# Performance work log

Measured on AMD Instinct MI355X. Metric: run time of the kernel, lower is better.

Reference implementation:

```python
import jax, jax.numpy as jnp
import numpy as np

D = 2048   # embed_dim
E = 128    # expand_ratio = head dim
H = D // E # num heads = 16
C = 64     # chunk size for the chunked linear-attention scan
EPS = 1e-6


def setup_inputs() -> dict:
    key = jax.random.key(0)
    ks = jax.random.split(key, 6)
    b, n = 2, 2048
    s = 0.02
    x = jax.random.normal(ks[0], (b, n, D), jnp.float32)
    Wq = (jax.random.normal(ks[1], (D, D), jnp.float32) * s)
    Wk = (jax.random.normal(ks[2], (D, D), jnp.float32) * s)
    Wv = (jax.random.normal(ks[3], (D, D), jnp.float32) * s)
    Wf = (jax.random.normal(ks[4], (D, H), jnp.float32) * s)
    Wo = (jax.random.normal(ks[5], (D, D), jnp.float32) * s)
    norm_w = jnp.ones((D,), jnp.float32)
    return {"x": x, "Wq": Wq, "Wk": Wk, "Wv": Wv, "Wf": Wf, "Wo": Wo, "norm_w": norm_w}


def _lightning_scalar_decay(q, k, v, ld):
    # q,k,v: [b,n,H,E], ld: [b,n,H] log decay per head per step.
    # Recurrence: S_t = exp(ld_t) * S_{t-1} + k_t^T v_t ; o_t = q_t @ S_t
    b, n, h, e = q.shape
    nc = n // C
    qc = q.reshape(b, nc, C, h, e)
    kc = k.reshape(b, nc, C, h, e)
    vc = v.reshape(b, nc, C, h, e)
    ldc = ld.reshape(b, nc, C, h)
    cum = jnp.cumsum(ldc, axis=2)          # inclusive within-chunk log decay [b,nc,C,h]
    tot = cum[:, :, -1, :]                 # [b,nc,h]

    # intra-chunk: scores[i,j] = (q_i . k_j) * exp(L_i - L_j), j <= i
    Lh = cum.transpose(0, 1, 3, 2)         # [b,nc,h,C]
    decay = jnp.exp(Lh[..., :, None] - Lh[..., None, :])  # [b,nc,h,C,C]
    mask = jnp.tril(jnp.ones((C, C), bool))
    scores = jnp.einsum('bmihe,bmjhe->bmhij', qc, kc) * decay
    scores = jnp.where(mask, scores, 0.0)
    o_intra = jnp.einsum('bmhij,bmjhe->bmihe', scores, vc)

    # inter-chunk: carried recurrent state S [b,h,e,e]
    def step(S, inp):
        q_c, k_c, v_c, cum_c, tot_c = inp  # [b,C,h,e],...,[b,C,h],[b,h]
        o = jnp.einsum('bihe,bhef->bihf', q_c * jnp.exp(cum_c)[..., None], S)
        kd = k_c * jnp.exp(tot_c[:, None, :] - cum_c)[..., None]
        S_new = S * jnp.exp(tot_c)[:, :, None, None] + jnp.einsum('bihe,bihf->bhef', kd, v_c)
        return S_new, o

    xs = (qc.transpose(1, 0, 2, 3, 4), kc.transpose(1, 0, 2, 3, 4),
          vc.transpose(1, 0, 2, 3, 4), cum.transpose(1, 0, 2, 3), tot.transpose(1, 0, 2))
    S0 = jnp.zeros((b, h, e, e), q.dtype)
    S_final, o_inter = jax.lax.scan(step, S0, xs)
    o_inter = o_inter.transpose(1, 0, 2, 3, 4)  # [b,nc,C,h,e]
    return (o_intra + o_inter).reshape(b, n, h * e), S_final


def reference(x, Wq, Wk, Wv, Wf, Wo, norm_w):
    b, n, d = x.shape
    q = jax.nn.silu(x @ Wq).reshape(b, n, H, E)
    k = jax.nn.silu(x @ Wk).reshape(b, n, H, E)
    v = (x @ Wv).reshape(b, n, H, E)
    ld = jax.nn.log_sigmoid(x @ Wf)  # [b,n,H]
    o, _ = _lightning_scalar_decay(q, k, v, ld)
    # RMSNorm over full embed dim
    o = o * jax.lax.rsqrt(jnp.mean(o * o, axis=-1, keepdims=True) + EPS) * norm_w
    return o @ Wo
```

## Files before the change

kernel.cpp:

```cpp
#include <hip/hip_runtime.h>
#include <hip/hip_bf16.h>
#include <stdint.h>

#define D_ 2048
#define E_ 128
#define H_ 16
#define NB_ 2
#define NSEQ_ 2048
#define NTOK_ 4096
#define NCH_ 32

typedef short bf16s;
typedef __attribute__((ext_vector_type(8))) short bf16x8;
typedef __attribute__((ext_vector_type(4))) float f32x4;

__device__ __forceinline__ short f2b(float f) {
  __hip_bfloat16 h = __float2bfloat16(f);
  return *reinterpret_cast<short*>(&h);
}
__device__ __forceinline__ float b2f(short s) {
  __hip_bfloat16 h;
  *reinterpret_cast<short*>(&h) = s;
  return __bfloat162float(h);
}

__device__ __forceinline__ void gload_lds16(const void* g, void* l) {
  __builtin_amdgcn_global_load_lds(
      (__attribute__((address_space(1))) void*)(const_cast<void*>(g)),
      (__attribute__((address_space(3))) void*)(l), 16, 0, 0);
}

__global__ __launch_bounds__(256)
void cvt_bf16(const float* __restrict__ x, bf16s* __restrict__ y) {
  const size_t i = (size_t)blockIdx.x * 256 + threadIdx.x;
  const float4 a = ((const float4*)x)[i * 2];
  const float4 b = ((const float4*)x)[i * 2 + 1];
  bf16x8 o;
  o[0] = f2b(a.x); o[1] = f2b(a.y); o[2] = f2b(a.z); o[3] = f2b(a.w);
  o[4] = f2b(b.x); o[5] = f2b(b.y); o[6] = f2b(b.z); o[7] = f2b(b.w);
  *(bf16x8*)&y[i * 8] = o;
}

__global__ __launch_bounds__(256)
void transpose_w(const float* __restrict__ Wq, const float* __restrict__ Wk,
                 const float* __restrict__ Wv, const float* __restrict__ Wo,
                 bf16s* __restrict__ WqT, bf16s* __restrict__ WkT,
                 bf16s* __restrict__ WvT, bf16s* __restrict__ WoT) {
  const float* src; bf16s* dst;
  if (blockIdx.z == 0)      { src = Wq; dst = WqT; }
  else if (blockIdx.z == 1) { src = Wk; dst = WkT; }
  else if (blockIdx.z == 2) { src = Wv; dst = WvT; }
  else                      { src = Wo; dst = WoT; }
  __shared__ float tile[64][65];
  const int n0 = blockIdx.x * 64, k0 = blockIdx.y * 64;
  const int t = threadIdx.x;
  const int tr = t >> 6, tc = t & 63;
#pragma unroll
  for (int rr = 0; rr < 16; ++rr) {
    const int row = rr * 4 + tr;
    tile[row][tc] = src[(size_t)(k0 + row) * D_ + n0 + tc];
  }
  __syncthreads();
#pragma unroll
  for (int rr = 0; rr < 16; ++rr) {
    const int row = rr * 4 + tr;
    dst[(size_t)(n0 + row) * D_ + k0 + tc] = f2b(tile[tc][row]);
  }
}

__global__ __launch_bounds__(256)
void ld_gemm(const float* __restrict__ x, const float* __restrict__ Wf,
             float* __restrict__ ldb) {
  const int t = threadIdx.x;
  const int col = t & 15;
  const int tok = blockIdx.x * 16 + (t >> 4);
  const float4* xr = (const float4*)(x + (size_t)tok * D_);
  float s = 0.f;
#pragma unroll 4
  for (int kk = 0; kk < D_ / 4; ++kk) {
    const float4 xv = xr[kk];
    const int k4 = kk * 4;
    s += xv.x * Wf[(k4 + 0) * H_ + col];
    s += xv.y * Wf[(k4 + 1) * H_ + col];
    s += xv.z * Wf[(k4 + 2) * H_ + col];
    s += xv.w * Wf[(k4 + 3) * H_ + col];
  }
  const float m = fminf(s, 0.f);
  ldb[(size_t)tok * H_ + col] = m - log1pf(__expf(-fabsf(s)));
}

template <typename OT>
__device__ __forceinline__ void gemm_body(const bf16s* __restrict__ A,
                                          const bf16s* __restrict__ Bt,
                                          OT* __restrict__ Cm, int bm, int bn,
                                          int act) {
  constexpr int BK = 64;
  __shared__ bf16s As[128 * BK];
  __shared__ bf16s Bs[128 * BK];
  const int t = threadIdx.x;
  const int w = t >> 6, l = t & 63;
  const int wm = w >> 1, wn = w & 1;
  const int lr = l & 15, lk = l >> 4;
  const int sr8 = l >> 3, sc = l & 7;
  const int cs = sc ^ sr8;
  f32x4 acc[4][4] = {};

  const size_t abase = (size_t)(bm * 128) * D_;
  const size_t bbase = (size_t)(bn * 128) * D_;

  for (int k0 = 0; k0 < D_; k0 += BK) {
    __syncthreads();
#pragma unroll
    for (int j = 0; j < 4; ++j) {
      const int row = w * 32 + j * 8;
      gload_lds16(&A[abase + (size_t)(row + sr8) * D_ + k0 + cs * 8],
                  &As[row * BK]);
      gload_lds16(&Bt[bbase + (size_t)(row + sr8) * D_ + k0 + cs * 8],
                  &Bs[row * BK]);
    }
    __syncthreads();
    bf16x8 af[4][2], bfr[4][2];
#pragma unroll
    for (int tm = 0; tm < 4; ++tm) {
      const int row = wm * 64 + tm * 16 + lr;
#pragma unroll
      for (int ks = 0; ks < 2; ++ks)
        af[tm][ks] =
            *(const bf16x8*)&As[row * BK + ((ks * 4 + lk) ^ (row & 7)) * 8];
    }
#pragma unroll
    for (int tn = 0; tn < 4; ++tn) {
      const int row = wn * 64 + tn * 16 + lr;
#pragma unroll
      for (int ks = 0; ks < 2; ++ks)
        bfr[tn][ks] =
            *(const bf16x8*)&Bs[row * BK + ((ks * 4 + lk) ^ (row & 7)) * 8];
    }
#pragma unroll
    for (int ks = 0; ks < 2; ++ks)
#pragma unroll
      for (int tm = 0; tm < 4; ++tm)
#pragma unroll
        for (int tn = 0; tn < 4; ++tn)
          acc[tm][tn] = __builtin_amdgcn_mfma_f32_16x16x32_bf16(
              af[tm][ks], bfr[tn][ks], acc[tm][tn], 0, 0, 0);
  }

#pragma unroll
  for (int tm = 0; tm < 4; ++tm) {
    const int rowb = bm * 128 + wm * 64 + tm * 16 + lk * 4;
#pragma unroll
    for (int tn = 0; tn < 4; ++tn) {
      const int col = bn * 128 + wn * 64 + tn * 16 + lr;
#pragma unroll
      for (int r = 0; r < 4; ++r) {
        float vv = acc[tm][tn][r];
        if (act) vv = vv / (1.f + __expf(-vv));
        if constexpr (sizeof(OT) == 2)
          Cm[(size_t)(rowb + r) * D_ + col] = f2b(vv);
        else
          Cm[(size_t)(rowb + r) * D_ + col] = vv;
      }
    }
  }
}

__global__ __launch_bounds__(256)
void gemm_qkv(const bf16s* __restrict__ xb, const bf16s* __restrict__ WqT,
              const bf16s* __restrict__ WkT, const bf16s* __restrict__ WvT,
              bf16s* __restrict__ qb, bf16s* __restrict__ kb,
              bf16s* __restrict__ vb) {
  const int orig = blockIdx.x;
  const int lin = (orig & 7) * 192 + (orig >> 3);
  const int bm = lin & 31;
  const int bnz = lin >> 5;
  const int z = bnz >> 4, bn = bnz & 15;
  const bf16s* Bt; bf16s* out; int act;
  if (z == 0)      { Bt = WqT; out = qb; act = 1; }
  else if (z == 1) { Bt = WkT; out = kb; act = 1; }
  else             { Bt = WvT; out = vb; act = 0; }
  gemm_body<bf16s>(xb, Bt, out, bm, bn, act);
}

__global__ __launch_bounds__(256)
void gemm_out(const bf16s* __restrict__ A, const bf16s* __restrict__ Bt,
              float* __restrict__ out) {
  const int orig = blockIdx.x;
  const int lin = (orig & 7) * 64 + (orig >> 3);
  const int bm = lin & 31;
  const int bn = lin >> 5;
  gemm_body<float>(A, Bt, out, bm, bn, 0);
}

__global__ __launch_bounds__(256)
void chunk_state(const bf16s* __restrict__ k, const bf16s* __restrict__ v,
                 const float* __restrict__ ldp, bf16s* __restrict__ Mbuf,
                 float* __restrict__ totb) {
  const int c = blockIdx.x, bh = blockIdx.y;
  const int b = bh >> 4, h = bh & 15;
  const int t = threadIdx.x;
  const int w = t >> 6, l = t & 63;
  const int lr = l & 15, lk = l >> 4;

  __shared__ bf16s Kt[64 * 128];
  __shared__ bf16s Vn[64 * 128];
  __shared__ bf16s KdT[128 * 64];
  __shared__ bf16s VtT[128 * 64];
  __shared__ float cumS[64];
  char* cKt = (char*)Kt; char* cVn = (char*)Vn;
  char* cKdT = (char*)KdT; char* cVtT = (char*)VtT;

  const size_t grow0 = (size_t)b * NSEQ_ + c * 64;
#pragma unroll
  for (int j = 0; j < 4; ++j) {
    const int lrow = w * 16 + j * 4 + (l >> 4);
    const int ck = (l & 15) ^ (lrow & 7);
    const size_t goff = (grow0 + lrow) * D_ + h * E_ + ck * 8;
    const int lbase = (w * 16 + j * 4) * 128;
    gload_lds16(&k[goff], &Kt[lbase]);
    gload_lds16(&v[goff], &Vn[lbase]);
  }
  if (w == 0) {
    float val = ldp[(grow0 + l) * H_ + h];
#pragma unroll
    for (int off = 1; off < 64; off <<= 1) {
      float pv = __shfl_up(val, off);
      if (l >= off) val += pv;
    }
    cumS[l] = val;
  }
  __syncthreads();
  const float tot = cumS[63];
  if (t == 0) totb[bh * NCH_ + c] = tot;

#pragma unroll
  for (int it = 0; it < 4; ++it) {
    const int task = t + it * 256;
    const int i = task >> 4, cx = task & 15;
    const int sb = i * 256 + ((cx * 16) ^ ((i & 7) << 4));
    bf16x8 vv = *(const bf16x8*)(cVn + sb);
    bf16x8 kk8 = *(const bf16x8*)(cKt + sb);
    const float sE = __expf(tot - cumS[i]);
#pragma unroll
    for (int jj = 0; jj < 8; ++jj) {
      const int e = cx * 8 + jj;
      const int db = e * 128 + ((i * 2) ^ ((e & 7) << 4));
      *(bf16s*)(cVtT + db) = vv[jj];
      *(bf16s*)(cKdT + db) = f2b(b2f(kk8[jj]) * sE);
    }
  }
  __syncthreads();

  const int wm = w >> 1, wn = w & 1;
  f32x4 acc[4][4] = {};
#pragma unroll
  for (int kk2 = 0; kk2 < 2; ++kk2) {
    const int cb = (kk2 * 32 + lk * 8) * 2;
    bf16x8 af[4], bfr[4];
#pragma unroll
    for (int tm = 0; tm < 4; ++tm) {
      const int fr = wm * 64 + tm * 16 + lr;
      af[tm] = *(const bf16x8*)(cVtT + fr * 128 + (cb ^ ((fr & 7) << 4)));
    }
#pragma unroll
    for (int tn = 0; tn < 4; ++tn) {
      const int er = wn * 64 + tn * 16 + lr;
      bfr[tn] = *(const bf16x8*)(cKdT + er * 128 + (cb ^ ((er & 7) << 4)));
    }
#pragma unroll
    for (int tm = 0; tm < 4; ++tm)
#pragma unroll
      for (int tn = 0; tn < 4; ++tn)
        acc[tm][tn] = __builtin_amdgcn_mfma_f32_16x16x32_bf16(
            af[tm], bfr[tn], acc[tm][tn], 0, 0, 0);
  }
  const size_t mb = (size_t)(bh * NCH_ + c) * 128 * 128;
#pragma unroll
  for (int tm = 0; tm < 4; ++tm) {
#pragma unroll
    for (int tn = 0; tn < 4; ++tn) {
#pragma unroll
      for (int r = 0; r < 4; ++r) {
        const int f = wm * 64 + tm * 16 + lk * 4 + r;
        const int e = wn * 64 + tn * 16 + lr;
        Mbuf[mb + f * 128 + e] = f2b(acc[tm][tn][r]);
      }
    }
  }
}

__global__ __launch_bounds__(256)
void state_scan(const bf16s* __restrict__ Mbuf, const float* __restrict__ totb,
                bf16s* __restrict__ Sbuf) {
  const int sl = blockIdx.x;
  const int bh = blockIdx.y;
  const int t = threadIdx.x;
  const int fr = sl * 16 + (t >> 4);
  const int e0 = (t & 15) * 8;
  const size_t base = ((size_t)(bh * NCH_) * 128 + fr) * 128 + e0;
  const size_t cstride = 128 * 128;
  float acc[8] = {};
  bf16x8 m = *(const bf16x8*)&Mbuf[base];
  for (int c = 0; c < NCH_; ++c) {
    bf16x8 sv;
#pragma unroll
    for (int j = 0; j < 8; ++j) sv[j] = f2b(acc[j]);
    *(bf16x8*)&Sbuf[base + (size_t)c * cstride] = sv;
    bf16x8 mn = m;
    if (c + 1 < NCH_) mn = *(const bf16x8*)&Mbuf[base + (size_t)(c + 1) * cstride];
    const float dt = __expf(totb[bh * NCH_ + c]);
#pragma unroll
    for (int j = 0; j < 8; ++j) acc[j] = acc[j] * dt + b2f(m[j]);
    m = mn;
  }
}

__global__ __launch_bounds__(256)
void attn_out(const bf16s* __restrict__ q, const bf16s* __restrict__ k,
              const bf16s* __restrict__ v, const float* __restrict__ ldp,
              const bf16s* __restrict__ Sbuf, bf16s* __restrict__ o) {
  const int c = blockIdx.x, bh = blockIdx.y;
  const int b = bh >> 4, h = bh & 15;
  const int t = threadIdx.x;
  const int w = t >> 6, l = t & 63;
  const int lr = l & 15, lk = l >> 4;

  __shared__ bf16s Qt[64 * 128];
  __shared__ bf16s Kt[64 * 128];
  __shared__ bf16s Vn[64 * 128];
  __shared__ bf16s VtT[128 * 64];
  __shared__ bf16s St[128 * 128];
  __shared__ bf16s Pm[64 * 64];
  __shared__ float cumS[64];
  char* cQt = (char*)Qt; char* cKt = (char*)Kt; char* cVn = (char*)Vn;
  char* cVtT = (char*)VtT; char* cSt = (char*)St; char* cPm = (char*)Pm;

  const size_t grow0 = (size_t)b * NSEQ_ + c * 64;
  const size_t sbase = (size_t)(bh * NCH_ + c) * 128 * 128;
#pragma unroll
  for (int j = 0; j < 4; ++j) {
    const int lrow = w * 16 + j * 4 + (l >> 4);
    const int ck = (l & 15) ^ (lrow & 7);
    const size_t goff = (grow0 + lrow) * D_ + h * E_ + ck * 8;
    const int lbase = (w * 16 + j * 4) * 128;
    gload_lds16(&q[goff], &Qt[lbase]);
    gload_lds16(&k[goff], &Kt[lbase]);
    gload_lds16(&v[goff], &Vn[lbase]);
  }
#pragma unroll
  for (int j = 0; j < 8; ++j) {
    const int lrow = w * 32 + j * 4 + (l >> 4);
    const int ck = (l & 15) ^ (lrow & 7);
    gload_lds16(&Sbuf[sbase + (size_t)lrow * 128 + ck * 8],
                &St[(w * 32 + j * 4) * 128]);
  }
  if (w == 0) {
    float val = ldp[(grow0 + l) * H_ + h];
#pragma unroll
    for (int off = 1; off < 64; off <<= 1) {
      float pv = __shfl_up(val, off);
      if (l >= off) val += pv;
    }
    cumS[l] = val;
  }
  __syncthreads();

#pragma unroll
  for (int it = 0; it < 4; ++it) {
    const int task = t + it * 256;
    const int i = task >> 4, cx = task & 15;
    const int sb = i * 256 + ((cx * 16) ^ ((i & 7) << 4));
    bf16x8 vv = *(const bf16x8*)(cVn + sb);
#pragma unroll
    for (int jj = 0; jj < 8; ++jj) {
      const int e = cx * 8 + jj;
      const int db = e * 128 + ((i * 2) ^ ((e & 7) << 4));
      *(bf16s*)(cVtT + db) = vv[jj];
    }
  }

  f32x4 accs[4] = {};
  f32x4 acco[8] = {};
#pragma unroll
  for (int kk = 0; kk < 4; ++kk) {
    const int cb = (kk * 32 + lk * 8) * 2;
    const int ar = w * 16 + lr;
    bf16x8 aq = *(const bf16x8*)(cQt + ar * 256 + (cb ^ ((ar & 7) << 4)));
#pragma unroll
    for (int tn = 0; tn < 4; ++tn) {
      const int br = tn * 16 + lr;
      bf16x8 bk = *(const bf16x8*)(cKt + br * 256 + (cb ^ ((br & 7) << 4)));
      accs[tn] = __builtin_amdgcn_mfma_f32_16x16x32_bf16(aq, bk, accs[tn], 0, 0, 0);
    }
#pragma unroll
    for (int tf = 0; tf < 8; ++tf) {
      const int sr = tf * 16 + lr;
      bf16x8 bs = *(const bf16x8*)(cSt + sr * 256 + (cb ^ ((sr & 7) << 4)));
      acco[tf] = __builtin_amdgcn_mfma_f32_16x16x32_bf16(aq, bs, acco[tf], 0, 0, 0);
    }
  }
#pragma unroll
  for (int r = 0; r < 4; ++r) {
    const float gI = __expf(cumS[w * 16 + lk * 4 + r]);
#pragma unroll
    for (int tf = 0; tf < 8; ++tf) acco[tf][r] *= gI;
  }
#pragma unroll
  for (int tn = 0; tn < 4; ++tn) {
    const int j = tn * 16 + lr;
    const float cj = cumS[j];
#pragma unroll
    for (int r = 0; r < 4; ++r) {
      const int i = w * 16 + lk * 4 + r;
      const float sv = (j <= i) ? accs[tn][r] * __expf(cumS[i] - cj) : 0.f;
      *(bf16s*)(cPm + i * 128 + ((j * 2) ^ ((i & 7) << 4))) = f2b(sv);
    }
  }
  __syncthreads();

#pragma unroll
  for (int kk2 = 0; kk2 < 2; ++kk2) {
    const int cb = (kk2 * 32 + lk * 8) * 2;
    const int pr = w * 16 + lr;
    bf16x8 ap = *(const bf16x8*)(cPm + pr * 128 + (cb ^ ((pr & 7) << 4)));
#pragma unroll
    for (int tf = 0; tf < 8; ++tf) {
      const int fr = tf * 16 + lr;
      bf16x8 bv = *(const bf16x8*)(cVtT + fr * 128 + (cb ^ ((fr & 7) << 4)));
      acco[tf] = __builtin_amdgcn_mfma_f32_16x16x32_bf16(ap, bv, acco[tf], 0, 0, 0);
    }
  }
#pragma unroll
  for (int tf = 0; tf < 8; ++tf) {
#pragma unroll
    for (int r = 0; r < 4; ++r) {
      const int i = w * 16 + lk * 4 + r;
      o[(grow0 + i) * D_ + h * E_ + tf * 16 + lr] = f2b(acco[tf][r]);
    }
  }
}

__global__ __launch_bounds__(256)
void rmsnorm(bf16s* __restrict__ o, const float* __restrict__ nw) {
  const int tok = blockIdx.x;
  const int t = threadIdx.x;
  bf16s* row = o + (size_t)tok * D_;
  bf16x8 vv = *(bf16x8*)&row[t * 8];
  float f[8];
  float s = 0.f;
#pragma unroll
  for (int j = 0; j < 8; ++j) { f[j] = b2f(vv[j]); s += f[j] * f[j]; }
#pragma unroll
  for (int off2 = 32; off2 > 0; off2 >>= 1) s += __shfl_down(s, off2);
  __shared__ float wsum[4];
  if ((t & 63) == 0) wsum[t >> 6] = s;
  __syncthreads();
  const float scale =
      rsqrtf((wsum[0] + wsum[1] + wsum[2] + wsum[3]) * (1.f / D_) + 1e-6f);
  bf16x8 ov;
#pragma unroll
  for (int j = 0; j < 8; ++j) ov[j] = f2b(f[j] * scale * nw[t * 8 + j]);
  *(bf16x8*)&row[t * 8] = ov;
}

extern "C" void kernel_launch(void* const* d_in, const int* in_sizes, int n_in,
                              void* d_out, int out_size, void* d_ws,
                              size_t ws_size, hipStream_t stream) {
  (void)in_sizes; (void)n_in; (void)out_size;
  const float* x  = (const float*)d_in[0];
  const float* Wq = (const float*)d_in[1];
  const float* Wk = (const float*)d_in[2];
  const float* Wv = (const float*)d_in[3];
  const float* Wf = (const float*)d_in[4];
  const float* Wo = (const float*)d_in[5];
  const float* nw = (const float*)d_in[6];
  float* out = (float*)d_out;

  char* ws = (char*)d_ws;
  const size_t MB = 1024 * 1024;
  bf16s* xb   = (bf16s*)(ws + 0);
  bf16s* WqT  = (bf16s*)(ws + 16 * MB);
  bf16s* WkT  = (bf16s*)(ws + 24 * MB);
  bf16s* WvT  = (bf16s*)(ws + 32 * MB);
  bf16s* Sbuf = (bf16s*)(ws + 0);
  float* totb = (float*)(ws + 32 * MB);
  bf16s* WoT  = (bf16s*)(ws + 40 * MB);
  bf16s* qb   = (bf16s*)(ws + 48 * MB);
  bf16s* kb   = (bf16s*)(ws + 64 * MB);
  bf16s* vb   = (bf16s*)(ws + 80 * MB);
  bf16s* ob   = (bf16s*)(ws + 96 * MB);
  bf16s* Mbuf = (bf16s*)(ws + 112 * MB);
  float* ldb  = (float*)(ws + 144 * MB);
  if (145 * MB > ws_size) return;

  cvt_bf16<<<NTOK_ * D_ / 8 / 256, 256, 0, stream>>>(x, xb);
  transpose_w<<<dim3(32, 32, 4), 256, 0, stream>>>(Wq, Wk, Wv, Wo, WqT, WkT,
                                                   WvT, WoT);
  ld_gemm<<<NTOK_ / 16, 256, 0, stream>>>(x, Wf, ldb);
  gemm_qkv<<<1536, 256, 0, stream>>>(xb, WqT, WkT, WvT, qb, kb, vb);
  chunk_state<<<dim3(NCH_, NB_ * H_), 256, 0, stream>>>(kb, vb, ldb, Mbuf, totb);
  state_scan<<<dim3(8, NB_ * H_), 256, 0, stream>>>(Mbuf, totb, Sbuf);
  attn_out<<<dim3(NCH_, NB_ * H_), 256, 0, stream>>>(qb, kb, vb, ldb, Sbuf, ob);
  rmsnorm<<<NTOK_, 256, 0, stream>>>(ob, nw);
  gemm_out<<<512, 256, 0, stream>>>(ob, WoT, out);
}
```

Before: 342.1 us.

## Fold RMSNorm into output GEMM, prefetch scan loads, read state directly

RMSNorm is split so a small kernel computes only the per-token inverse RMS. The norm weight is folded into the transposed Wo, and the output GEMM epilogue multiplies each row by the stored scale, so the normalized activations are no longer written back. The state scan now prefetches four chunks ahead and keeps the decay totals in shared memory. attn_out reads the S fragments straight from global memory instead of staging them in LDS. Risks: the un-normalized bf16 activations now feed the GEMM, which changes rounding slightly, and the direct global reads of S may be less efficient than the staged copy.

After: 312.7 us. 1.09x faster.

```diff
diff --git a/kernel.cpp b/kernel.cpp
--- a/kernel.cpp
+++ b/kernel.cpp
@@ -44,8 +44,9 @@
 __global__ __launch_bounds__(256)
 void transpose_w(const float* __restrict__ Wq, const float* __restrict__ Wk,
                  const float* __restrict__ Wv, const float* __restrict__ Wo,
-                 bf16s* __restrict__ WqT, bf16s* __restrict__ WkT,
-                 bf16s* __restrict__ WvT, bf16s* __restrict__ WoT) {
+                 const float* __restrict__ nw, bf16s* __restrict__ WqT,
+                 bf16s* __restrict__ WkT, bf16s* __restrict__ WvT,
+                 bf16s* __restrict__ WoT) {
   const float* src; bf16s* dst;
   if (blockIdx.z == 0)      { src = Wq; dst = WqT; }
   else if (blockIdx.z == 1) { src = Wk; dst = WkT; }
@@ -61,10 +62,11 @@
     tile[row][tc] = src[(size_t)(k0 + row) * D_ + n0 + tc];
   }
   __syncthreads();
+  const float wk = (blockIdx.z == 3) ? nw[k0 + tc] : 1.f;
 #pragma unroll
   for (int rr = 0; rr < 16; ++rr) {
     const int row = rr * 4 + tr;
-    dst[(size_t)(n0 + row) * D_ + k0 + tc] = f2b(tile[tc][row]);
+    dst[(size_t)(n0 + row) * D_ + k0 + tc] = f2b(tile[tc][row] * wk);
   }
 }
 
@@ -93,7 +95,7 @@
 __device__ __forceinline__ void gemm_body(const bf16s* __restrict__ A,
                                           const bf16s* __restrict__ Bt,
                                           OT* __restrict__ Cm, int bm, int bn,
-                                          int act) {
+                                          int act, const float* __restrict__ rs) {
   constexpr int BK = 64;
   __shared__ bf16s As[128 * BK];
   __shared__ bf16s Bs[128 * BK];
@@ -156,10 +158,12 @@
       for (int r = 0; r < 4; ++r) {
         float vv = acc[tm][tn][r];
         if (act) vv = vv / (1.f + __expf(-vv));
-        if constexpr (sizeof(OT) == 2)
+        if constexpr (sizeof(OT) == 2) {
           Cm[(size_t)(rowb + r) * D_ + col] = f2b(vv);
-        else
+        } else {
+          vv *= rs[rowb + r];
           Cm[(size_t)(rowb + r) * D_ + col] = vv;
+        }
       }
     }
   }
@@ -179,17 +183,17 @@
   if (z == 0)      { Bt = WqT; out = qb; act = 1; }
   else if (z == 1) { Bt = WkT; out = kb; act = 1; }
   else             { Bt = WvT; out = vb; act = 0; }
-  gemm_body<bf16s>(xb, Bt, out, bm, bn, act);
+  gemm_body<bf16s>(xb, Bt, out, bm, bn, act, nullptr);
 }
 
 __global__ __launch_bounds__(256)
 void gemm_out(const bf16s* __restrict__ A, const bf16s* __restrict__ Bt,
-              float* __restrict__ out) {
+              const float* __restrict__ rs, float* __restrict__ out) {
   const int orig = blockIdx.x;
   const int lin = (orig & 7) * 64 + (orig >> 3);
   const int bm = lin & 31;
   const int bn = lin >> 5;
-  gemm_body<float>(A, Bt, out, bm, bn, 0);
+  gemm_body<float>(A, Bt, out, bm, bn, 0, rs);
 }
 
 __global__ __launch_bounds__(256)
@@ -299,19 +303,32 @@
   const int e0 = (t & 15) * 8;
   const size_t base = ((size_t)(bh * NCH_) * 128 + fr) * 128 + e0;
   const size_t cstride = 128 * 128;
+  __shared__ float tots[NCH_];
+  if (t < NCH_) tots[t] = totb[bh * NCH_ + t];
+  __syncthreads();
   float acc[8] = {};
-  bf16x8 m = *(const bf16x8*)&Mbuf[base];
+  bf16x8 m0 = *(const bf16x8*)&Mbuf[base + 0 * cstride];
+  bf16x8 m1 = *(const bf16x8*)&Mbuf[base + 1 * cstride];
+  bf16x8 m2 = *(const bf16x8*)&Mbuf[base + 2 * cstride];
+  bf16x8 m3 = *(const bf16x8*)&Mbuf[base + 3 * cstride];
+#pragma unroll
   for (int c = 0; c < NCH_; ++c) {
     bf16x8 sv;
 #pragma unroll
     for (int j = 0; j < 8; ++j) sv[j] = f2b(acc[j]);
     *(bf16x8*)&Sbuf[base + (size_t)c * cstride] = sv;
-    bf16x8 mn = m;
-    if (c + 1 < NCH_) mn = *(const bf16x8*)&Mbuf[base + (size_t)(c + 1) * cstride];
-    const float dt = __expf(totb[bh * NCH_ + c]);
-#pragma unroll
-    for (int j = 0; j < 8; ++j) acc[j] = acc[j] * dt + b2f(m[j]);
-    m = mn;
+    const bf16x8 mc = ((c & 3) == 0) ? m0 : ((c & 3) == 1) ? m1
+                     : ((c & 3) == 2) ? m2 : m3;
+    const float dt = __expf(tots[c]);
+#pragma unroll
+    for (int j = 0; j < 8; ++j) acc[j] = acc[j] * dt + b2f(mc[j]);
+    if (c + 4 < NCH_) {
+      const bf16x8 mn = *(const bf16x8*)&Mbuf[base + (size_t)(c + 4) * cstride];
+      if ((c & 3) == 0) m0 = mn;
+      else if ((c & 3) == 1) m1 = mn;
+      else if ((c & 3) == 2) m2 = mn;
+      else m3 = mn;
+    }
   }
 }
 
@@ -329,14 +346,14 @@
   __shared__ bf16s Kt[64 * 128];
   __shared__ bf16s Vn[64 * 128];
   __shared__ bf16s VtT[128 * 64];
-  __shared__ bf16s St[128 * 128];
   __shared__ bf16s Pm[64 * 64];
   __shared__ float cumS[64];
   char* cQt = (char*)Qt; char* cKt = (char*)Kt; char* cVn = (char*)Vn;
-  char* cVtT = (char*)VtT; char* cSt = (char*)St; char* cPm = (char*)Pm;
+  char* cVtT = (char*)VtT; char* cPm = (char*)Pm;
 
   const size_t grow0 = (size_t)b * NSEQ_ + c * 64;
   const size_t sbase = (size_t)(bh * NCH_ + c) * 128 * 128;
+  const bf16x8* Sp = (const bf16x8*)&Sbuf[sbase];
 #pragma unroll
   for (int j = 0; j < 4; ++j) {
     const int lrow = w * 16 + j * 4 + (l >> 4);
@@ -347,13 +364,6 @@
     gload_lds16(&k[goff], &Kt[lbase]);
     gload_lds16(&v[goff], &Vn[lbase]);
   }
-#pragma unroll
-  for (int j = 0; j < 8; ++j) {
-    const int lrow = w * 32 + j * 4 + (l >> 4);
-    const int ck = (l & 15) ^ (lrow & 7);
-    gload_lds16(&Sbuf[sbase + (size_t)lrow * 128 + ck * 8],
-                &St[(w * 32 + j * 4) * 128]);
-  }
   if (w == 0) {
     float val = ldp[(grow0 + l) * H_ + h];
 #pragma unroll
@@ -394,8 +404,7 @@
     }
 #pragma unroll
     for (int tf = 0; tf < 8; ++tf) {
-      const int sr = tf * 16 + lr;
-      bf16x8 bs = *(const bf16x8*)(cSt + sr * 256 + (cb ^ ((sr & 7) << 4)));
+      bf16x8 bs = Sp[(tf * 16 + lr) * 16 + kk * 4 + lk];
       acco[tf] = __builtin_amdgcn_mfma_f32_16x16x32_bf16(aq, bs, acco[tf], 0, 0, 0);
     }
   }
@@ -441,26 +450,21 @@
 }
 
 __global__ __launch_bounds__(256)
-void rmsnorm(bf16s* __restrict__ o, const float* __restrict__ nw) {
+void rms_scale(const bf16s* __restrict__ o, float* __restrict__ sout) {
   const int tok = blockIdx.x;
   const int t = threadIdx.x;
-  bf16s* row = o + (size_t)tok * D_;
-  bf16x8 vv = *(bf16x8*)&row[t * 8];
-  float f[8];
+  bf16x8 vv = *(const bf16x8*)&o[(size_t)tok * D_ + t * 8];
   float s = 0.f;
 #pragma unroll
-  for (int j = 0; j < 8; ++j) { f[j] = b2f(vv[j]); s += f[j] * f[j]; }
+  for (int j = 0; j < 8; ++j) { const float f = b2f(vv[j]); s += f * f; }
 #pragma unroll
   for (int off2 = 32; off2 > 0; off2 >>= 1) s += __shfl_down(s, off2);
   __shared__ float wsum[4];
   if ((t & 63) == 0) wsum[t >> 6] = s;
   __syncthreads();
-  const float scale =
-      rsqrtf((wsum[0] + wsum[1] + wsum[2] + wsum[3]) * (1.f / D_) + 1e-6f);
-  bf16x8 ov;
-#pragma unroll
-  for (int j = 0; j < 8; ++j) ov[j] = f2b(f[j] * scale * nw[t * 8 + j]);
-  *(bf16x8*)&row[t * 8] = ov;
+  if (t == 0)
+    sout[tok] = rsqrtf((wsum[0] + wsum[1] + wsum[2] + wsum[3]) * (1.f / D_) +
+                       1e-6f);
 }
 
 extern "C" void kernel_launch(void* const* d_in, const int* in_sizes, int n_in,
@@ -491,16 +495,17 @@
   bf16s* ob   = (bf16s*)(ws + 96 * MB);
   bf16s* Mbuf = (bf16s*)(ws + 112 * MB);
   float* ldb  = (float*)(ws + 144 * MB);
-  if (145 * MB > ws_size) return;
+  float* rsb  = (float*)(ws + 145 * MB);
+  if (146 * MB > ws_size) return;
 
   cvt_bf16<<<NTOK_ * D_ / 8 / 256, 256, 0, stream>>>(x, xb);
-  transpose_w<<<dim3(32, 32, 4), 256, 0, stream>>>(Wq, Wk, Wv, Wo, WqT, WkT,
-                                                   WvT, WoT);
+  transpose_w<<<dim3(32, 32, 4), 256, 0, stream>>>(Wq, Wk, Wv, Wo, nw, WqT,
+                                                   WkT, WvT, WoT);
   ld_gemm<<<NTOK_ / 16, 256, 0, stream>>>(x, Wf, ldb);
   gemm_qkv<<<1536, 256, 0, stream>>>(xb, WqT, WkT, WvT, qb, kb, vb);
   chunk_state<<<dim3(NCH_, NB_ * H_), 256, 0, stream>>>(kb, vb, ldb, Mbuf, totb);
   state_scan<<<dim3(8, NB_ * H_), 256, 0, stream>>>(Mbuf, totb, Sbuf);
   attn_out<<<dim3(NCH_, NB_ * H_), 256, 0, stream>>>(qb, kb, vb, ldb, Sbuf, ob);
-  rmsnorm<<<NTOK_, 256, 0, stream>>>(ob, nw);
-  gemm_out<<<512, 256, 0, stream>>>(ob, WoT, out);
-}
+  rms_scale<<<NTOK_, 256, 0, stream>>>(ob, rsb);
+  gemm_out<<<512, 256, 0, stream>>>(ob, WoT, rsb, out);
+}
```
